# Kernel tuning notes

Measured on AMD Instinct MI355X. Metric: run time of the kernel, lower is better.

The kernel has to match this reference:

```python
import jax, jax.numpy as jnp
import numpy as np

N_NODES = 100000
N_EDGES = 1000000
F_IN = 256
HID = 256
HID2 = 128
N_CLS = 2


def setup_inputs() -> dict:
    key = jax.random.key(0)
    ks = jax.random.split(key, 8)
    x = jax.random.normal(ks[0], (N_NODES, F_IN), dtype=jnp.float32)
    edge_index = jax.random.randint(ks[1], (2, N_EDGES), 0, N_NODES, dtype=jnp.int64)
    s = lambda k, shp: jax.random.normal(k, shp, dtype=jnp.float32) / np.sqrt(shp[0])
    return {
        "x": x,
        "edge_index": edge_index,
        "W1l": s(ks[2], (F_IN, HID)),
        "W1r": s(ks[3], (F_IN, HID)),
        "b1": jnp.zeros((HID,), jnp.float32),
        "W2l": s(ks[4], (HID, HID2)),
        "W2r": s(ks[5], (HID, HID2)),
        "b2": jnp.zeros((HID2,), jnp.float32),
        "Wc": s(ks[6], (HID2, N_CLS)),
        "bc": jnp.zeros((N_CLS,), jnp.float32),
    }


def _sage_conv(x, src, dst, deg_inv, Wl, Wr, b):
    # mean-aggregate neighbor (source) features at each destination node
    msg = x[src]                                              # [E, F]
    agg = jax.ops.segment_sum(msg, dst, num_segments=N_NODES)  # [N, F]
    mean = agg * deg_inv[:, None]                             # zero for isolated nodes
    return mean @ Wl + b + x @ Wr


def reference(x, edge_index, W1l, W1r, b1, W2l, W2r, b2, Wc, bc):
    src, dst = edge_index[0], edge_index[1]
    cnt = jax.ops.segment_sum(jnp.ones((N_EDGES,), x.dtype), dst, num_segments=N_NODES)
    deg_inv = jnp.where(cnt > 0, 1.0 / jnp.maximum(cnt, 1.0), 0.0)
    h = jax.nn.relu(_sage_conv(x, src, dst, deg_inv, W1l, W1r, b1))   # dropout is identity in eval
    h = jax.nn.relu(_sage_conv(h, src, dst, deg_inv, W2l, W2r, b2))
    logits = h @ Wc + bc
    return jax.nn.log_softmax(logits, axis=1)
```

## Files before the change

kernel.cpp:

```cpp
#include <hip/hip_runtime.h>
#include <hip/hip_bf16.h>

#define NN 100000
#define NE 1000000
#define MPAD 100096

typedef __attribute__((ext_vector_type(8))) short bf16x8;
typedef __attribute__((ext_vector_type(4))) float f32x4;
typedef __attribute__((ext_vector_type(8))) unsigned short us8;

static __device__ __forceinline__ float bf2f(unsigned short u){
  unsigned int x = ((unsigned int)u) << 16;
  return __uint_as_float(x);
}
static __device__ __forceinline__ unsigned short f2bf(float f){
  unsigned int x = __float_as_uint(f);
  unsigned int r = (x + 0x7fffu + ((x >> 16) & 1u)) >> 16;
  return (unsigned short)r;
}
static __device__ __forceinline__ void gld16(const void* g, void* l){
  __builtin_amdgcn_global_load_lds((const __attribute__((address_space(1))) void*)g,
                                   (__attribute__((address_space(3))) void*)l, 16, 0, 0);
}


__global__ void k_degree(const int* __restrict__ dst, int* __restrict__ cnt, int E){
  int e = blockIdx.x * blockDim.x + threadIdx.x;
  if (e < E) atomicAdd(&cnt[dst[e]], 1);
}

__global__ void k_chunk_sum(const int* __restrict__ cnt, int* __restrict__ partials, int N){
  __shared__ int sw[16];
  int b = blockIdx.x, t = threadIdx.x;
  int i = b * 1024 + t;
  int v = (i < N) ? cnt[i] : 0;
  #pragma unroll
  for (int off = 32; off; off >>= 1) v += __shfl_xor(v, off);
  int lane = t & 63, w = t >> 6;
  if (lane == 0) sw[w] = v;
  __syncthreads();
  if (t < 16){
    int s = sw[t];
    #pragma unroll
    for (int off = 8; off; off >>= 1) s += __shfl_xor(s, off);
    if (t == 0) partials[b] = s;
  }
}

__global__ void k_scan_partials(const int* __restrict__ partials, int* __restrict__ bases, int nchunk){
  if (threadIdx.x == 0 && blockIdx.x == 0){
    int run = 0;
    for (int j = 0; j < nchunk; j++){ bases[j] = run; run += partials[j]; }
  }
}

__global__ void k_chunk_scan(const int* __restrict__ cnt, const int* __restrict__ bases,
                             int* __restrict__ offs, int* __restrict__ cursor,
                             float* __restrict__ deginv, int N){
  __shared__ int sd[1024];
  int b = blockIdx.x, t = threadIdx.x;
  int i = b * 1024 + t;
  int v = (i < N) ? cnt[i] : 0;
  sd[t] = v;
  __syncthreads();
  for (int off = 1; off < 1024; off <<= 1){
    int x = (t >= off) ? sd[t - off] : 0;
    __syncthreads();
    sd[t] += x;
    __syncthreads();
  }
  if (i < N){
    int excl = bases[b] + sd[t] - v;
    offs[i] = excl;
    cursor[i] = excl;
    deginv[i] = (v > 0) ? (1.0f / (float)v) : 0.0f;
  }
}

__global__ void k_fill(const int* __restrict__ src, const int* __restrict__ dst,
                       int* __restrict__ cursor, int* __restrict__ csr, int E){
  int e = blockIdx.x * blockDim.x + threadIdx.x;
  if (e < E){
    int p = atomicAdd(&cursor[dst[e]], 1);
    csr[p] = src[e];
  }
}


__global__ void k_cvt(const float* __restrict__ x, unsigned short* __restrict__ xb){
  size_t i = ((size_t)blockIdx.x * 256 + threadIdx.x) * 8;
  if (i >= (size_t)MPAD * 256) return;
  int row = (int)(i >> 8);
  us8 o;
  if (row < NN){
    const float4* p = (const float4*)(x + i);
    float4 a = p[0], b = p[1];
    o[0]=f2bf(a.x); o[1]=f2bf(a.y); o[2]=f2bf(a.z); o[3]=f2bf(a.w);
    o[4]=f2bf(b.x); o[5]=f2bf(b.y); o[6]=f2bf(b.z); o[7]=f2bf(b.w);
  } else {
    #pragma unroll
    for (int j = 0; j < 8; j++) o[j] = 0;
  }
  *(us8*)(xb + i) = o;
}


__global__ void k_prep_w(const float* __restrict__ W1l, const float* __restrict__ W1r,
                         const float* __restrict__ W2l, const float* __restrict__ W2r,
                         unsigned short* __restrict__ Bt1, unsigned short* __restrict__ Bt2){
  int i = blockIdx.x * 256 + threadIdx.x;
  if (i < 512 * 256){
    int n = i >> 8, k = i & 255;
    float v = (n < 256) ? W1l[k * 256 + n] : W1r[k * 256 + (n - 256)];
    Bt1[n * 256 + k] = f2bf(v);
  }
  if (i < 256 * 256){
    int n = i >> 8, k = i & 255;
    float v = (n < 128) ? W2l[k * 128 + n] : W2r[k * 128 + (n - 128)];
    Bt2[n * 256 + k] = f2bf(v);
  }
}


__global__ __launch_bounds__(256)
void k_gemm(const unsigned short* __restrict__ A,
            const unsigned short* __restrict__ Bt,
            unsigned short* __restrict__ C,
            int Nout)
{
  __shared__ __align__(16) unsigned short lA[128 * 64];
  __shared__ __align__(16) unsigned short lB[128 * 64];
  const int t = threadIdx.x;
  const int lane = t & 63, wid = t >> 6;
  const int wm = wid >> 1, wn = wid & 1;
  const int m0 = blockIdx.x * 128;
  const int n0 = blockIdx.y * 128;

  f32x4 acc[4][4] = {};

  const int strow = wid * 32 + (lane >> 3);
  const int sc    = (lane & 7) ^ ((lane >> 3) & 7);

  for (int kt = 0; kt < 4; ++kt){
    __syncthreads();
    #pragma unroll
    for (int s4 = 0; s4 < 4; ++s4){
      int row = strow + s4 * 8;
      gld16(A  + (size_t)(m0 + row) * 256 + kt * 64 + sc * 8, &lA[(wid * 4 + s4) * 512]);
      gld16(Bt + (size_t)(n0 + row) * 256 + kt * 64 + sc * 8, &lB[(wid * 4 + s4) * 512]);
    }
    __syncthreads();
    #pragma unroll
    for (int ks = 0; ks < 2; ++ks){
      bf16x8 av[4], bv[4];
      const int kc = ks * 4 + (lane >> 4);
      #pragma unroll
      for (int m = 0; m < 4; m++){
        int r = wm * 64 + m * 16 + (lane & 15);
        av[m] = *(const bf16x8*)&lA[r * 64 + ((kc ^ (r & 7)) << 3)];
      }
      #pragma unroll
      for (int n = 0; n < 4; n++){
        int c = wn * 64 + n * 16 + (lane & 15);
        bv[n] = *(const bf16x8*)&lB[c * 64 + ((kc ^ (c & 7)) << 3)];
      }
      #pragma unroll
      for (int m = 0; m < 4; m++)
        #pragma unroll
        for (int n = 0; n < 4; n++)
          acc[m][n] = __builtin_amdgcn_mfma_f32_16x16x32_bf16(av[m], bv[n], acc[m][n], 0, 0, 0);
    }
  }

  const int crow0 = m0 + wm * 64 + (lane >> 4) * 4;
  const int ccol0 = n0 + wn * 64 + (lane & 15);
  #pragma unroll
  for (int m = 0; m < 4; m++){
    #pragma unroll
    for (int r = 0; r < 4; r++){
      size_t rowoff = (size_t)(crow0 + m * 16 + r) * Nout;
      #pragma unroll
      for (int n = 0; n < 4; n++)
        C[rowoff + ccol0 + n * 16] = f2bf(acc[m][n][r]);
    }
  }
}


__global__ void k_agg1(const unsigned short* __restrict__ C1,
                       const float* __restrict__ b1,
                       const int* __restrict__ offs, const int* __restrict__ cnt,
                       const float* __restrict__ deginv,
                       const int* __restrict__ csr,
                       unsigned short* __restrict__ h, int N)
{
  int wv = threadIdx.x >> 6, lane = threadIdx.x & 63;
  int n = blockIdx.x * 4 + wv;
  if (n >= N) return;
  int beg = offs[n], d = cnt[n];
  const int g = lane >> 5;
  const int cl = lane & 31;

  float acc[8];
  #pragma unroll
  for (int k = 0; k < 8; k++) acc[k] = 0.f;

  for (int w0 = 0; w0 < d; w0 += 64){
    int wlen = min(d - w0, 64);
    int idx = 0;
    if (lane < wlen) idx = csr[beg + w0 + lane];
    int nIter = (wlen + 7) >> 3;
    for (int t = 0; t < nIter; t++){
      int e0 = t * 8 + g;
      int s0 = __shfl(idx, e0);
      int s1 = __shfl(idx, e0 + 2);
      int s2 = __shfl(idx, e0 + 4);
      int s3 = __shfl(idx, e0 + 6);
      us8 v0 = *(const us8*)(C1 + (size_t)s0 * 512 + cl * 8);
      us8 v1 = *(const us8*)(C1 + (size_t)s1 * 512 + cl * 8);
      us8 v2 = *(const us8*)(C1 + (size_t)s2 * 512 + cl * 8);
      us8 v3 = *(const us8*)(C1 + (size_t)s3 * 512 + cl * 8);
      if (e0 < wlen){
        #pragma unroll
        for (int k = 0; k < 8; k++) acc[k] += bf2f(v0[k]);
      }
      if (e0 + 2 < wlen){
        #pragma unroll
        for (int k = 0; k < 8; k++) acc[k] += bf2f(v1[k]);
      }
      if (e0 + 4 < wlen){
        #pragma unroll
        for (int k = 0; k < 8; k++) acc[k] += bf2f(v2[k]);
      }
      if (e0 + 6 < wlen){
        #pragma unroll
        for (int k = 0; k < 8; k++) acc[k] += bf2f(v3[k]);
      }
    }
  }
  #pragma unroll
  for (int k = 0; k < 8; k++) acc[k] += __shfl_xor(acc[k], 32);

  if (lane < 32){
    float di = deginv[n];
    us8 rv = *(const us8*)(C1 + (size_t)n * 512 + 256 + cl * 8);
    float4 b0 = *(const float4*)(b1 + cl * 8);
    float4 b4 = *(const float4*)(b1 + cl * 8 + 4);
    float bb[8] = {b0.x, b0.y, b0.z, b0.w, b4.x, b4.y, b4.z, b4.w};
    us8 o;
    #pragma unroll
    for (int k = 0; k < 8; k++)
      o[k] = f2bf(fmaxf(acc[k] * di + bf2f(rv[k]) + bb[k], 0.f));
    *(us8*)(h + (size_t)n * 256 + cl * 8) = o;
  }
}


__global__ void k_agg2cls(const unsigned short* __restrict__ C2,
                          const float* __restrict__ b2,
                          const float* __restrict__ Wc,
                          const float* __restrict__ bc,
                          const int* __restrict__ offs, const int* __restrict__ cnt,
                          const float* __restrict__ deginv,
                          const int* __restrict__ csr,
                          float* __restrict__ out, int N)
{
  int wv = threadIdx.x >> 6, lane = threadIdx.x & 63;
  int n = blockIdx.x * 4 + wv;
  if (n >= N) return;
  int beg = offs[n], d = cnt[n];
  const int g = lane >> 4;
  const int cl = lane & 15;

  float acc[8];
  #pragma unroll
  for (int k = 0; k < 8; k++) acc[k] = 0.f;

  for (int w0 = 0; w0 < d; w0 += 64){
    int wlen = min(d - w0, 64);
    int idx = 0;
    if (lane < wlen) idx = csr[beg + w0 + lane];
    int nIter = (wlen + 15) >> 4;
    for (int t = 0; t < nIter; t++){
      int e0 = t * 16 + g;
      int s0 = __shfl(idx, e0);
      int s1 = __shfl(idx, e0 + 4);
      int s2 = __shfl(idx, e0 + 8);
      int s3 = __shfl(idx, e0 + 12);
      us8 v0 = *(const us8*)(C2 + (size_t)s0 * 256 + cl * 8);
      us8 v1 = *(const us8*)(C2 + (size_t)s1 * 256 + cl * 8);
      us8 v2 = *(const us8*)(C2 + (size_t)s2 * 256 + cl * 8);
      us8 v3 = *(const us8*)(C2 + (size_t)s3 * 256 + cl * 8);
      if (e0 < wlen){
        #pragma unroll
        for (int k = 0; k < 8; k++) acc[k] += bf2f(v0[k]);
      }
      if (e0 + 4 < wlen){
        #pragma unroll
        for (int k = 0; k < 8; k++) acc[k] += bf2f(v1[k]);
      }
      if (e0 + 8 < wlen){
        #pragma unroll
        for (int k = 0; k < 8; k++) acc[k] += bf2f(v2[k]);
      }
      if (e0 + 12 < wlen){
        #pragma unroll
        for (int k = 0; k < 8; k++) acc[k] += bf2f(v3[k]);
      }
    }
  }
  #pragma unroll
  for (int k = 0; k < 8; k++){
    acc[k] += __shfl_xor(acc[k], 16);
    acc[k] += __shfl_xor(acc[k], 32);
  }

  float di = deginv[n];
  us8 rv = *(const us8*)(C2 + (size_t)n * 256 + 128 + cl * 8);
  float4 b0 = *(const float4*)(b2 + cl * 8);
  float4 b4 = *(const float4*)(b2 + cl * 8 + 4);
  float bb[8] = {b0.x, b0.y, b0.z, b0.w, b4.x, b4.y, b4.z, b4.w};
  float p0 = 0.f, p1 = 0.f;
  #pragma unroll
  for (int k = 0; k < 8; k += 2){
    float h0 = fmaxf(acc[k]     * di + bf2f(rv[k])     + bb[k],     0.f);
    float h1 = fmaxf(acc[k + 1] * di + bf2f(rv[k + 1]) + bb[k + 1], 0.f);
    float4 w = *(const float4*)(Wc + (cl * 8 + k) * 2);
    p0 += h0 * w.x + h1 * w.z;
    p1 += h0 * w.y + h1 * w.w;
  }
  #pragma unroll
  for (int off = 8; off; off >>= 1){
    p0 += __shfl_xor(p0, off);
    p1 += __shfl_xor(p1, off);
  }
  if (lane == 0){
    float z0 = p0 + bc[0], z1 = p1 + bc[1];
    float m = fmaxf(z0, z1);
    float lse = m + logf(expf(z0 - m) + expf(z1 - m));
    out[(size_t)n * 2 + 0] = z0 - lse;
    out[(size_t)n * 2 + 1] = z1 - lse;
  }
}


extern "C" void kernel_launch(void* const* d_in, const int* in_sizes, int n_in,
                              void* d_out, int out_size, void* d_ws, size_t ws_size,
                              hipStream_t stream)
{
  const float* x   = (const float*)d_in[0];
  const int*   ei  = (const int*)d_in[1];
  const float* W1l = (const float*)d_in[2];
  const float* W1r = (const float*)d_in[3];
  const float* b1  = (const float*)d_in[4];
  const float* W2l = (const float*)d_in[5];
  const float* W2r = (const float*)d_in[6];
  const float* b2  = (const float*)d_in[7];
  const float* Wc  = (const float*)d_in[8];
  const float* bc  = (const float*)d_in[9];
  float* out = (float*)d_out;

  const int N = NN, E = NE;
  const int* src = ei;
  const int* dst = ei + E;

  char* ws = (char*)d_ws;
  size_t off = 0;
  auto alloc = [&](size_t bytes) -> void* {
    void* p = ws + off;
    off += (bytes + 255) & ~(size_t)255;
    return p;
  };
  int*   cnt      = (int*)alloc((size_t)N * 4);
  int*   offs     = (int*)alloc((size_t)N * 4);
  int*   cursor   = (int*)alloc((size_t)N * 4);
  float* deginv   = (float*)alloc((size_t)N * 4);
  int*   partials = (int*)alloc(1024);
  int*   bases    = (int*)alloc(1024);
  int*   csr      = (int*)alloc((size_t)E * 4);
  unsigned short* Bt1 = (unsigned short*)alloc((size_t)512 * 256 * 2);
  unsigned short* Bt2 = (unsigned short*)alloc((size_t)256 * 256 * 2);
  unsigned short* xb  = (unsigned short*)alloc((size_t)MPAD * 256 * 2);
  unsigned short* C1  = (unsigned short*)alloc((size_t)MPAD * 512 * 2);

  unsigned short* h  = xb;
  unsigned short* C2 = C1;

  (void)in_sizes; (void)n_in; (void)out_size; (void)ws_size;

  hipMemsetAsync(cnt, 0, (size_t)N * 4, stream);

  int nchunk = (N + 1023) / 1024;
  k_degree<<<(E + 255) / 256, 256, 0, stream>>>(dst, cnt, E);
  k_chunk_sum<<<nchunk, 1024, 0, stream>>>(cnt, partials, N);
  k_scan_partials<<<1, 64, 0, stream>>>(partials, bases, nchunk);
  k_chunk_scan<<<nchunk, 1024, 0, stream>>>(cnt, bases, offs, cursor, deginv, N);
  k_fill<<<(E + 255) / 256, 256, 0, stream>>>(src, dst, cursor, csr, E);

  k_cvt<<<MPAD / 8, 256, 0, stream>>>(x, xb);
  k_prep_w<<<512, 256, 0, stream>>>(W1l, W1r, W2l, W2r, Bt1, Bt2);

  {
    dim3 g(MPAD / 128, 512 / 128);
    k_gemm<<<g, 256, 0, stream>>>(xb, Bt1, C1, 512);
  }
  k_agg1<<<N / 4, 256, 0, stream>>>(C1, b1, offs, cnt, deginv, csr, h, N);

  {
    dim3 g(MPAD / 128, 256 / 128);
    k_gemm<<<g, 256, 0, stream>>>(h, Bt2, C2, 256);
  }
  k_agg2cls<<<N / 4, 256, 0, stream>>>(C2, b2, Wc, bc, offs, cnt, deginv, csr, out, N);
}
```

Baseline: 368.4 us.

## Fuse partial scan into chunk scan, XCD-aware GEMM tiling, deeper gather unroll

Removes the single-thread partial-scan kernel and has each chunk-scan block reduce the preceding partials in shared memory, which saves a launch and a serial loop. The GEMMs move to a 1D grid remapped so consecutive M tiles and all their N tiles land on the same XCD, aiming for better L2 reuse of A rows. Both aggregation kernels now issue 8 gathered row loads per iteration instead of 4, putting more memory requests in flight. This raises register pressure in the aggregation kernels and adds some early-exit padding blocks in the GEMM.

```diff
diff --git a/kernel.cpp b/kernel.cpp
--- a/kernel.cpp
+++ b/kernel.cpp
@@ -4,6 +4,8 @@
 #define NN 100000
 #define NE 1000000
 #define MPAD 100096
+#define MT   782
+#define MTP  784
 
 typedef __attribute__((ext_vector_type(8))) short bf16x8;
 typedef __attribute__((ext_vector_type(4))) float f32x4;
@@ -17,6 +19,10 @@
   unsigned int x = __float_as_uint(f);
   unsigned int r = (x + 0x7fffu + ((x >> 16) & 1u)) >> 16;
   return (unsigned short)r;
+}
+static __device__ __forceinline__ void addv(float* acc, us8 v){
+  #pragma unroll
+  for (int k = 0; k < 8; k++) acc[k] += bf2f(v[k]);
 }
 static __device__ __forceinline__ void gld16(const void* g, void* l){
   __builtin_amdgcn_global_load_lds((const __attribute__((address_space(1))) void*)g,
@@ -47,22 +53,23 @@
   }
 }
 
-__global__ void k_scan_partials(const int* __restrict__ partials, int* __restrict__ bases, int nchunk){
-  if (threadIdx.x == 0 && blockIdx.x == 0){
-    int run = 0;
-    for (int j = 0; j < nchunk; j++){ bases[j] = run; run += partials[j]; }
-  }
-}
-
-__global__ void k_chunk_scan(const int* __restrict__ cnt, const int* __restrict__ bases,
+__global__ void k_chunk_scan(const int* __restrict__ cnt, const int* __restrict__ partials,
+                             int nchunk,
                              int* __restrict__ offs, int* __restrict__ cursor,
                              float* __restrict__ deginv, int N){
   __shared__ int sd[1024];
+  __shared__ int sp[128];
   int b = blockIdx.x, t = threadIdx.x;
+  if (t < 128) sp[t] = (t < b && t < nchunk) ? partials[t] : 0;
   int i = b * 1024 + t;
   int v = (i < N) ? cnt[i] : 0;
   sd[t] = v;
   __syncthreads();
+  #pragma unroll
+  for (int off = 64; off; off >>= 1){
+    if (t < off) sp[t] += sp[t + off];
+    __syncthreads();
+  }
   for (int off = 1; off < 1024; off <<= 1){
     int x = (t >= off) ? sd[t - off] : 0;
     __syncthreads();
@@ -70,7 +77,7 @@
     __syncthreads();
   }
   if (i < N){
-    int excl = bases[b] + sd[t] - v;
+    int excl = sp[0] + sd[t] - v;
     offs[i] = excl;
     cursor[i] = excl;
     deginv[i] = (v > 0) ? (1.0f / (float)v) : 0.0f;
@@ -122,19 +129,26 @@
 }
 
 
+template<int NTL2>
 __global__ __launch_bounds__(256)
 void k_gemm(const unsigned short* __restrict__ A,
             const unsigned short* __restrict__ Bt,
-            unsigned short* __restrict__ C,
-            int Nout)
+            unsigned short* __restrict__ C)
 {
+  const int bid = blockIdx.x;
+  const int xcd = bid & 7, j = bid >> 3;
+  const int mt  = xcd * (MTP / 8) + (j >> NTL2);
+  if (mt >= MT) return;
+  const int nt  = j & ((1 << NTL2) - 1);
+  const int m0  = mt * 128;
+  const int n0  = nt * 128;
+  const int Nout = 128 << NTL2;
+
   __shared__ __align__(16) unsigned short lA[128 * 64];
   __shared__ __align__(16) unsigned short lB[128 * 64];
   const int t = threadIdx.x;
   const int lane = t & 63, wid = t >> 6;
   const int wm = wid >> 1, wn = wid & 1;
-  const int m0 = blockIdx.x * 128;
-  const int n0 = blockIdx.y * 128;
 
   f32x4 acc[4][4] = {};
 
@@ -209,33 +223,33 @@
     int wlen = min(d - w0, 64);
     int idx = 0;
     if (lane < wlen) idx = csr[beg + w0 + lane];
-    int nIter = (wlen + 7) >> 3;
+    int nIter = (wlen + 15) >> 4;
     for (int t = 0; t < nIter; t++){
-      int e0 = t * 8 + g;
+      int e0 = t * 16 + g;
       int s0 = __shfl(idx, e0);
       int s1 = __shfl(idx, e0 + 2);
       int s2 = __shfl(idx, e0 + 4);
       int s3 = __shfl(idx, e0 + 6);
+      int s4 = __shfl(idx, e0 + 8);
+      int s5 = __shfl(idx, e0 + 10);
+      int s6 = __shfl(idx, e0 + 12);
+      int s7 = __shfl(idx, e0 + 14);
       us8 v0 = *(const us8*)(C1 + (size_t)s0 * 512 + cl * 8);
       us8 v1 = *(const us8*)(C1 + (size_t)s1 * 512 + cl * 8);
       us8 v2 = *(const us8*)(C1 + (size_t)s2 * 512 + cl * 8);
       us8 v3 = *(const us8*)(C1 + (size_t)s3 * 512 + cl * 8);
-      if (e0 < wlen){
-        #pragma unroll
-        for (int k = 0; k < 8; k++) acc[k] += bf2f(v0[k]);
-      }
-      if (e0 + 2 < wlen){
-        #pragma unroll
-        for (int k = 0; k < 8; k++) acc[k] += bf2f(v1[k]);
-      }
-      if (e0 + 4 < wlen){
-        #pragma unroll
-        for (int k = 0; k < 8; k++) acc[k] += bf2f(v2[k]);
-      }
-      if (e0 + 6 < wlen){
-        #pragma unroll
-        for (int k = 0; k < 8; k++) acc[k] += bf2f(v3[k]);
-      }
+      us8 v4 = *(const us8*)(C1 + (size_t)s4 * 512 + cl * 8);
+      us8 v5 = *(const us8*)(C1 + (size_t)s5 * 512 + cl * 8);
+      us8 v6 = *(const us8*)(C1 + (size_t)s6 * 512 + cl * 8);
+      us8 v7 = *(const us8*)(C1 + (size_t)s7 * 512 + cl * 8);
+      if (e0 < wlen)      addv(acc, v0);
+      if (e0 + 2 < wlen)  addv(acc, v1);
+      if (e0 + 4 < wlen)  addv(acc, v2);
+      if (e0 + 6 < wlen)  addv(acc, v3);
+      if (e0 + 8 < wlen)  addv(acc, v4);
+      if (e0 + 10 < wlen) addv(acc, v5);
+      if (e0 + 12 < wlen) addv(acc, v6);
+      if (e0 + 14 < wlen) addv(acc, v7);
     }
   }
   #pragma unroll
@@ -280,33 +294,33 @@
     int wlen = min(d - w0, 64);
     int idx = 0;
     if (lane < wlen) idx = csr[beg + w0 + lane];
-    int nIter = (wlen + 15) >> 4;
+    int nIter = (wlen + 31) >> 5;
     for (int t = 0; t < nIter; t++){
-      int e0 = t * 16 + g;
+      int e0 = t * 32 + g;
       int s0 = __shfl(idx, e0);
       int s1 = __shfl(idx, e0 + 4);
       int s2 = __shfl(idx, e0 + 8);
       int s3 = __shfl(idx, e0 + 12);
+      int s4 = __shfl(idx, e0 + 16);
+      int s5 = __shfl(idx, e0 + 20);
+      int s6 = __shfl(idx, e0 + 24);
+      int s7 = __shfl(idx, e0 + 28);
       us8 v0 = *(const us8*)(C2 + (size_t)s0 * 256 + cl * 8);
       us8 v1 = *(const us8*)(C2 + (size_t)s1 * 256 + cl * 8);
       us8 v2 = *(const us8*)(C2 + (size_t)s2 * 256 + cl * 8);
       us8 v3 = *(const us8*)(C2 + (size_t)s3 * 256 + cl * 8);
-      if (e0 < wlen){
-        #pragma unroll
-        for (int k = 0; k < 8; k++) acc[k] += bf2f(v0[k]);
-      }
-      if (e0 + 4 < wlen){
-        #pragma unroll
-        for (int k = 0; k < 8; k++) acc[k] += bf2f(v1[k]);
-      }
-      if (e0 + 8 < wlen){
-        #pragma unroll
-        for (int k = 0; k < 8; k++) acc[k] += bf2f(v2[k]);
-      }
-      if (e0 + 12 < wlen){
-        #pragma unroll
-        for (int k = 0; k < 8; k++) acc[k] += bf2f(v3[k]);
-      }
+      us8 v4 = *(const us8*)(C2 + (size_t)s4 * 256 + cl * 8);
+      us8 v5 = *(const us8*)(C2 + (size_t)s5 * 256 + cl * 8);
+      us8 v6 = *(const us8*)(C2 + (size_t)s6 * 256 + cl * 8);
+      us8 v7 = *(const us8*)(C2 + (size_t)s7 * 256 + cl * 8);
+      if (e0 < wlen)      addv(acc, v0);
+      if (e0 + 4 < wlen)  addv(acc, v1);
+      if (e0 + 8 < wlen)  addv(acc, v2);
+      if (e0 + 12 < wlen) addv(acc, v3);
+      if (e0 + 16 < wlen) addv(acc, v4);
+      if (e0 + 20 < wlen) addv(acc, v5);
+      if (e0 + 24 < wlen) addv(acc, v6);
+      if (e0 + 28 < wlen) addv(acc, v7);
     }
   }
   #pragma unroll
@@ -376,7 +390,6 @@
   int*   cursor   = (int*)alloc((size_t)N * 4);
   float* deginv   = (float*)alloc((size_t)N * 4);
   int*   partials = (int*)alloc(1024);
-  int*   bases    = (int*)alloc(1024);
   int*   csr      = (int*)alloc((size_t)E * 4);
   unsigned short* Bt1 = (unsigned short*)alloc((size_t)512 * 256 * 2);
   unsigned short* Bt2 = (unsigned short*)alloc((size_t)256 * 256 * 2);
@@ -393,22 +406,15 @@
   int nchunk = (N + 1023) / 1024;
   k_degree<<<(E + 255) / 256, 256, 0, stream>>>(dst, cnt, E);
   k_chunk_sum<<<nchunk, 1024, 0, stream>>>(cnt, partials, N);
-  k_scan_partials<<<1, 64, 0, stream>>>(partials, bases, nchunk);
-  k_chunk_scan<<<nchunk, 1024, 0, stream>>>(cnt, bases, offs, cursor, deginv, N);
+  k_chunk_scan<<<nchunk, 1024, 0, stream>>>(cnt, partials, nchunk, offs, cursor, deginv, N);
   k_fill<<<(E + 255) / 256, 256, 0, stream>>>(src, dst, cursor, csr, E);
 
   k_cvt<<<MPAD / 8, 256, 0, stream>>>(x, xb);
   k_prep_w<<<512, 256, 0, stream>>>(W1l, W1r, W2l, W2r, Bt1, Bt2);
 
-  {
-    dim3 g(MPAD / 128, 512 / 128);
-    k_gemm<<<g, 256, 0, stream>>>(xb, Bt1, C1, 512);
-  }
+  k_gemm<2><<<MTP * 4, 256, 0, stream>>>(xb, Bt1, C1);
   k_agg1<<<N / 4, 256, 0, stream>>>(C1, b1, offs, cnt, deginv, csr, h, N);
 
-  {
-    dim3 g(MPAD / 128, 256 / 128);
-    k_gemm<<<g, 256, 0, stream>>>(h, Bt2, C2, 256);
-  }
+  k_gemm<1><<<MTP * 2, 256, 0, stream>>>(h, Bt2, C2);
   k_agg2cls<<<N / 4, 256, 0, stream>>>(C2, b2, Wc, bc, offs, cnt, deginv, csr, out, N);
 }
```

Result: faster. 359.7 us (-2.4%).
